# Kernel optimization log

Measured on AMD Instinct MI355X. Metric: run time of the kernel, lower is better.

Reference implementation:

```python
import jax, jax.numpy as jnp
import numpy as np

DISPS = (8, 8, 4, 2)
STRIDES = (2, 1, 1, 1)
DG = 4      # deformable groups
PAD = 1     # (kernel_size-1)//2 for k=3
KH = KW = 3


def pointwise_corr(f1, f2, disp, stride):
    """Windowed pointwise cross-correlation.
    f1, f2: [B, C, H, W]. Returns [B, (2d+1)^2, H, W], dy-major shift order,
    displacement step = stride, normalized by channel count.
    """
    B, C, H, W = f1.shape
    pad = disp * stride
    f2p = jnp.pad(f2, ((0, 0), (0, 0), (pad, pad), (pad, pad)))
    rng = np.arange(2 * disp + 1) * stride
    shifts = np.stack(np.meshgrid(rng, rng, indexing='ij'), -1).reshape(-1, 2)
    shifts = jnp.asarray(shifts, jnp.int32)

    def one(s):
        f2s = jax.lax.dynamic_slice(f2p, (0, 0, s[0], s[1]), (B, C, H, W))
        return jnp.sum(f1 * f2s, axis=1) / C   # [B, H, W]

    corr = jax.vmap(one)(shifts)               # [K2, B, H, W]
    return jnp.transpose(corr, (1, 0, 2, 3))


def bilinear_sample(img, y, x):
    """img: [cg, H, W]; y, x: [K2, H, W] float sample coords.
    Zero outside boundaries (deform-conv semantics). Returns [cg, K2, H, W]."""
    cg, H, W = img.shape
    y0 = jnp.floor(y); x0 = jnp.floor(x)
    wy = y - y0;       wx = x - x0
    y0i = y0.astype(jnp.int32); x0i = x0.astype(jnp.int32)

    def gather(iy, ix):
        valid = (iy >= 0) & (iy < H) & (ix >= 0) & (ix < W)
        v = img[:, jnp.clip(iy, 0, H - 1), jnp.clip(ix, 0, W - 1)]  # [cg,K2,H,W]
        return v * valid.astype(img.dtype)

    v00 = gather(y0i,     x0i)
    v01 = gather(y0i,     x0i + 1)
    v10 = gather(y0i + 1, x0i)
    v11 = gather(y0i + 1, x0i + 1)
    return (v00 * (1 - wy) * (1 - wx) + v01 * (1 - wy) * wx
            + v10 * wy * (1 - wx) + v11 * wy * wx)


def deform_conv(x, offset, weight, dg, pad):
    """Deformable conv v1, stride 1. x: [N,C,H,W]; offset: [N, dg*2*K2, H, W]
    (per group, per kernel point, (dy,dx)); weight: [O, C, kh, kw]."""
    N, C, H, W = x.shape
    O, _, kh, kw = weight.shape
    K2 = kh * kw
    cg = C // dg
    off = offset.reshape(N, dg, K2, 2, H, W)
    ky, kx = np.meshgrid(np.arange(kh), np.arange(kw), indexing='ij')
    ky = jnp.asarray(ky.reshape(-1), jnp.float32)
    kx = jnp.asarray(kx.reshape(-1), jnp.float32)
    gy = jnp.arange(H, dtype=jnp.float32)
    gx = jnp.arange(W, dtype=jnp.float32)
    base_y = ky[:, None, None] - pad + gy[None, :, None]   # [K2,H,1]
    base_x = kx[:, None, None] - pad + gx[None, None, :]   # [K2,1,W]
    ys = base_y[None, None] + off[:, :, :, 0]              # [N,dg,K2,H,W]
    xs = base_x[None, None] + off[:, :, :, 1]
    xg = x.reshape(N, dg, cg, H, W)
    sampled = jax.vmap(jax.vmap(bilinear_sample))(xg, ys, xs)  # [N,dg,cg,K2,H,W]
    w = weight.reshape(O, dg, cg, K2)
    return jnp.einsum('ogck,ngckhw->nohw', w, sampled)


def _forward_single(x, w_off, w_adapt, disp, stride):
    T, B, C, H, W = x.shape
    corrs = [pointwise_corr(x[t], x[t - 1], disp, stride) for t in range(1, T)]
    corr = jnp.concatenate(corrs, axis=0)                   # [(T-1)*B, K2, H, W]
    offset = jnp.einsum('ok,bkhw->bohw', w_off, corr)       # 1x1 conv, no bias
    feat_in = x[1:].reshape((T - 1) * B, C, H, W)
    feat = jax.nn.relu(deform_conv(feat_in, offset, w_adapt, DG, PAD))
    return jnp.concatenate([x[0], feat], axis=0)            # [T*B, C, H, W]


def setup_inputs() -> dict:
    key = jax.random.key(0)
    ks = jax.random.split(key, 12)
    shapes = [(2, 2, 256, 64, 64), (2, 2, 256, 32, 32),
              (2, 2, 256, 16, 16), (2, 2, 256, 8, 8)]
    d = {}
    for i, s in enumerate(shapes):
        d[f"x{i}"] = jax.random.normal(ks[i], s, jnp.float32)
    for i, disp in enumerate(DISPS):
        K2 = (2 * disp + 1) ** 2
        d[f"w_off{i}"] = 0.01 * jax.random.normal(ks[4 + i], (DG * 2 * KH * KW, K2), jnp.float32)
        d[f"w_adapt{i}"] = 0.01 * jax.random.normal(ks[8 + i], (256, 256, KH, KW), jnp.float32)
    return d


def reference(x0, x1, x2, x3, w_off0, w_off1, w_off2, w_off3,
              w_adapt0, w_adapt1, w_adapt2, w_adapt3):
    xs = [x0, x1, x2, x3]
    w_offs = [w_off0, w_off1, w_off2, w_off3]
    w_adapts = [w_adapt0, w_adapt1, w_adapt2, w_adapt3]
    outs = [_forward_single(xs[l], w_offs[l], w_adapts[l], DISPS[l], STRIDES[l])
            for l in range(4)]
    return tuple(outs)
```

## Files before the change

### kernel.cpp

```cpp
#include <hip/hip_runtime.h>

typedef unsigned int u32;
typedef unsigned short u16;
typedef _Float16 f16x2 __attribute__((ext_vector_type(2)));
typedef _Float16 f16x8 __attribute__((ext_vector_type(8)));
typedef __bf16 bf16x8 __attribute__((ext_vector_type(8)));
typedef float f32x4 __attribute__((ext_vector_type(4)));

static __device__ __forceinline__ f16x2 bch(u32 u) { return __builtin_bit_cast(f16x2, u); }


__global__ __launch_bounds__(256) void prep_kernel(
    const float* __restrict__ x0, const float* __restrict__ x1,
    const float* __restrict__ x2, const float* __restrict__ x3,
    const float* __restrict__ w0, const float* __restrict__ w1,
    const float* __restrict__ w2, const float* __restrict__ w3,
    u32* __restrict__ xq, u16* __restrict__ A, float* __restrict__ offs,
    float* __restrict__ out)
{
  __shared__ u32 plds[32 * 65];
  int bx = blockIdx.x, t = threadIdx.x;
  if (bx < 3060) {
    int i = bx * 256 + t;
    if (i < 783360) offs[i] = 0.f;
    return;
  }
  if (bx < 4420) {
    int local = bx - 3060;
    const float* xs; int lvlb, lgW, lgnch;
    if (local < 1024)      { xs = x0; lvlb = 0;       lgW = 6; lgnch = 6; }
    else if (local < 1280) { xs = x1; lvlb = 2097152; lgW = 5; lgnch = 4; local -= 1024; }
    else if (local < 1344) { xs = x2; lvlb = 2621440; lgW = 4; lgnch = 2; local -= 1280; }
    else                   { xs = x3; lvlb = 2752512; lgW = 3; lgnch = 0; local -= 1344; }
    int HW = 1 << (2 * lgW);
    int hc = local & ((1 << lgnch) - 1);
    int g  = (local >> lgnch) & 3;
    int tb = local >> (lgnch + 2);
    int hw0 = hc * 64;
    int lane = t & 63, qd = t >> 6;
#pragma unroll
    for (int j = 0; j < 8; ++j) {
      int cpw = qd * 8 + j;
      int c = tb * 256 + g * 64 + cpw * 2;
      const float* s = xs + (size_t)c * HW + hw0 + lane;
      float f0 = s[0], f1 = s[HW];
      f16x2 h; h[0] = (_Float16)f0; h[1] = (_Float16)f1;
      plds[cpw * 65 + lane] = __builtin_bit_cast(u32, h);
    }
    __syncthreads();
    u32* dst = xq + lvlb + (size_t)(tb * 4 + g) * HW * 32 + (size_t)hw0 * 32;
#pragma unroll
    for (int j = 0; j < 8; ++j) {
      int ow = j * 256 + t;
      int hwl = ow >> 5, ww = ow & 31;
      dst[(size_t)hwl * 32 + ww] = plds[ww * 65 + hwl];
    }
    return;
  }
  if (bx < 13636) {
    int i = (bx - 4420) * 256 + t;
    if (i >= 2359296) return;
    int lv = i / 589824;
    const float* w = (lv == 0) ? w0 : (lv == 1) ? w1 : (lv == 2) ? w2 : w3;
    int local = i - lv * 589824;
    int o = local / 2304;
    int k = local - o * 2304;
    int g = k / 576;
    int r = k - g * 576;
    int p = r >> 6;
    int c = r & 63;
    float v = w[(size_t)(o * 256 + g * 64 + c) * 9 + p];
    __bf16 bv = (__bf16)v;
    A[i] = __builtin_bit_cast(u16, bv);
    return;
  }
  {
    int i = (bx - 13636) * 256 + t;
    const float* xs; int base, dstb;
    if (i < 2097152)      { xs = x0; base = 0;       dstb = 0; }
    else if (i < 2621440) { xs = x1; base = 2097152; dstb = 4194304; }
    else if (i < 2752512) { xs = x2; base = 2621440; dstb = 5242880; }
    else if (i < 2785280) { xs = x3; base = 2752512; dstb = 5505024; }
    else return;
    int local = i - base;
    out[(size_t)dstb + local] = xs[local];
  }
}

__global__ __launch_bounds__(256) void corr_mfma_kernel(const u32* __restrict__ xq, float* __restrict__ corr)
{
  __shared__ __align__(16) u32 lds[8192];
  int t = threadIdx.x, bx = blockIdx.x;

  if (bx >= 1472) {
    int gw = ((bx - 1472) * 256 + t) >> 6;
    int lane = t & 63;
    int cs = lane >> 4, hwi = lane & 15;
    int obase = gw * 16;
    int K2, R, DISP, lgW, xqlb, crb, rel;
    if (obase < 41472)      { K2 = 81; R = 9; DISP = 4; lgW = 4; xqlb = 2621440; crb = 2959360; rel = obase; }
    else if (obase < 44672) { K2 = 25; R = 5; DISP = 2; lgW = 3; xqlb = 2752512; crb = 3000832; rel = obase - 41472; }
    else return;
    int W = 1 << lgW, HW = W * W;
    int hw = (rel & (HW - 1)) + hwi;
    int rr = rel >> (2 * lgW);
    int k = rr % K2, b = rr / K2;
    int h = hw >> lgW, wc = hw & (W - 1);
    int dy = k / R - DISP, dx = k % R - DISP;
    int h2 = h + dy, w2 = wc + dx;
    float a = 0.f;
    if ((u32)h2 < (u32)W && (u32)w2 < (u32)W) {
      const u32* q1 = xq + xqlb + ((size_t)((2 + b) * 4 + cs) * HW + hw) * 32;
      const u32* q0 = xq + xqlb + ((size_t)(b * 4 + cs) * HW + (h2 * W + w2)) * 32;
#pragma unroll 8
      for (int j = 0; j < 32; ++j)
        a = __builtin_amdgcn_fdot2(bch(q1[j]), bch(q0[j]), a, false);
    }
    a += __shfl_xor(a, 16);
    a += __shfl_xor(a, 32);
    if (cs == 0) corr[crb + rel + hwi] = a * 0.00390625f;
    return;
  }

  int sbx = (bx & 7) * 184 + (bx >> 3);
  int l = t & 63, w = t >> 6;
  int lvl, b, y, kq, lgW, W, HW, xqlb, crb;
  if (sbx < 1152) { lvl = 0; int r = sbx;        kq = r % 9; r /= 9; y = r & 63; b = r >> 6;
                    lgW = 6; W = 64; HW = 4096; xqlb = 0;       crb = 0; }
  else            { lvl = 1; int r = sbx - 1152; kq = r % 5; r /= 5; y = r & 31; b = r >> 5;
                    lgW = 5; W = 32; HW = 1024; xqlb = 2097152; crb = 2367488; }
  int par, qy, storeok;
  if (lvl == 0) { int rr = w >> 1; par = w & 1; qy = (kq < 8) ? 2 * kq + rr : 16;
                  storeok = !(kq == 8 && w >= 2); }
  else          { par = 0; qy = 4 * kq + w; storeok = (qy <= 16); if (qy > 16) qy = 16; }
  int rowY = (lvl == 0) ? (y + 2 * qy - 16) : (y + qy - 8);
  int f1words = (lvl == 0) ? 1024 : 512;
  int tb1 = 2 + b, tb0 = b;

  bool f1do = (lvl == 0) || (w < 2);
  u32 f1_lo; int f1_dw;
  {
    int G = w * 64 + l;
    int px = G >> 2, s = G & 3;
    int i = px & 31;
    int pari = px >> 5;
    int x = (lvl == 0) ? (2 * i + pari) : px;
    int cg = (s ^ ((i & 3) ^ ((i >> 2) & 3))) & 3;
    f1_lo = (u32)(xqlb + (y * W + x) * 32 + cg * 4);
    f1_dw = w * 256;
  }
  u32 f2_lo[3], f2_mask[3]; int f2_dw[3];
#pragma unroll
  for (int q = 0; q < 3; ++q) {
    int F = q * 64 + l;
    int jp = F >> 2, s = F & 3;
    int cg = (s ^ ((jp & 3) ^ ((jp >> 2) & 3))) & 3;
    int xs = (lvl == 0) ? (2 * (jp - 8) + par) : (jp - 8);
    bool valid = ((u32)xs < (u32)W) && ((u32)rowY < (u32)W);
    f2_lo[q]   = valid ? (u32)(xqlb + (rowY * W + xs) * 32 + cg * 4) : 6968960u;
    f2_mask[q] = valid ? 0xFFFFFFFFu : 0u;
    f2_dw[q]   = f1words + w * 768 + q * 256;
  }
  int lr = l & 15, lk = l >> 4;
  int aoff[2], boff[3];
#pragma unroll
  for (int it = 0; it < 2; ++it) {
    int iA = it * 16 + lr;
    int px = ((lvl == 0) ? par * 32 : 0) + iA;
    int phys = (lk ^ ((iA & 3) ^ ((iA >> 2) & 3))) & 3;
    aoff[it] = (px * 16 + phys * 4) * 4;
  }
#pragma unroll
  for (int T = 0; T < 3; ++T) {
    int jp = T * 16 + lr;
    int phys = (lk ^ ((jp & 3) ^ ((jp >> 2) & 3))) & 3;
    boff[T] = (f1words + w * 768 + jp * 16 + phys * 4) * 4;
  }

  f32x4 acc0 = {0,0,0,0}, acc1 = {0,0,0,0}, acc2 = {0,0,0,0}, acc3 = {0,0,0,0};

  auto issue = [&](int ch, int sel) {
    int g2 = ch >> 1, hf = ch & 1;
    u32 cb1 = ((u32)(tb1 * 4 + g2) * (u32)HW) * 32u + (u32)hf * 16u;
    u32 cb0 = ((u32)(tb0 * 4 + g2) * (u32)HW) * 32u + (u32)hf * 16u;
    u32* lb = &lds[sel * 4096];
    if (f1do)
      __builtin_amdgcn_global_load_lds(xq + cb1 + f1_lo, lb + f1_dw, 16, 0, 0);
#pragma unroll
    for (int q = 0; q < 3; ++q)
      __builtin_amdgcn_global_load_lds(xq + ((cb0 & f2_mask[q]) + f2_lo[q]), lb + f2_dw[q], 16, 0, 0);
  };

  issue(0, 0);
#pragma unroll 1
  for (int ch = 0; ch < 8; ++ch) {
    int sel = ch & 1;
    asm volatile("s_waitcnt vmcnt(0)" ::: "memory");
    asm volatile("s_barrier" ::: "memory");
    __builtin_amdgcn_sched_barrier(0);
    if (ch < 7) issue(ch + 1, sel ^ 1);
    const char* lb = (const char*)&lds[sel * 4096];
    f16x8 A0 = *(const f16x8*)(lb + aoff[0]);
    f16x8 A1 = *(const f16x8*)(lb + aoff[1]);
    f16x8 B0 = *(const f16x8*)(lb + boff[0]);
    f16x8 B1 = *(const f16x8*)(lb + boff[1]);
    f16x8 B2 = *(const f16x8*)(lb + boff[2]);
    acc0 = __builtin_amdgcn_mfma_f32_16x16x32_f16(A0, B0, acc0, 0, 0, 0);
    acc1 = __builtin_amdgcn_mfma_f32_16x16x32_f16(A0, B1, acc1, 0, 0, 0);
    acc2 = __builtin_amdgcn_mfma_f32_16x16x32_f16(A1, B1, acc2, 0, 0, 0);
    acc3 = __builtin_amdgcn_mfma_f32_16x16x32_f16(A1, B2, acc3, 0, 0, 0);
  }

  if (!storeok) return;
  const float sc = 0.00390625f;
#pragma unroll
  for (int tile = 0; tile < 4; ++tile) {
    int it = (tile >= 2) ? 1 : 0;
    int T  = (tile == 0) ? 0 : (tile == 3) ? 2 : 1;
    f32x4 av = (tile == 0) ? acc0 : (tile == 1) ? acc1 : (tile == 2) ? acc2 : acc3;
    int jp = T * 16 + lr;
#pragma unroll
    for (int jj = 0; jj < 4; ++jj) {
      int i = it * 16 + lk * 4 + jj;
      int qx = jp - i;
      if (qx >= 0 && qx <= 16) {
        int xo = (lvl == 0) ? (2 * i + par) : i;
        int k = qy * 17 + qx;
        corr[crb + (size_t)(b * 289 + k) * HW + y * W + xo] = av[jj] * sc;
      }
    }
  }
}

__global__ __launch_bounds__(256) void offset_kernel(
    const float* __restrict__ corr,
    const float* __restrict__ wo0, const float* __restrict__ wo1,
    const float* __restrict__ wo2, const float* __restrict__ wo3,
    float* __restrict__ offs)
{
  int t = threadIdx.x, bx = blockIdx.x;
  int kc = bx % 6;
  int unit = bx / 6;
  int og = unit & 3;
  int pb = unit >> 2;

  int lgW, K2, crb, ofb, pbl;
  const float* wo;
  if (pb < 32)      { pbl = pb;      lgW = 6; K2 = 289; crb = 0;       ofb = 0;      wo = wo0; }
  else if (pb < 40) { pbl = pb - 32; lgW = 5; K2 = 289; crb = 2367488; ofb = 589824; wo = wo1; }
  else if (pb < 42) { pbl = pb - 40; lgW = 4; K2 = 81;  crb = 2959360; ofb = 737280; wo = wo2; }
  else              { pbl = 0;       lgW = 3; K2 = 25;  crb = 3000832; ofb = 774144; wo = wo3; }
  int HW = 1 << (2 * lgW);
  int pxg = pbl * 256 + t;
  if (lgW == 3 && t >= 128) return;
  int b = pxg >> (2 * lgW);
  int hw = pxg & (HW - 1);

  int kchunk = (K2 + 5) / 6;
  int klo = kc * kchunk;
  int khi = klo + kchunk; if (khi > K2) khi = K2;
  if (klo >= khi) return;

  const float* cr = corr + crb + (size_t)b * K2 * HW + hw;
  const float* wp = wo + (size_t)og * 18 * K2;
  float acc[18];
#pragma unroll
  for (int j = 0; j < 18; ++j) acc[j] = 0.f;
#pragma unroll 2
  for (int k = klo; k < khi; ++k) {
    float cv = cr[(size_t)k * HW];
#pragma unroll
    for (int j = 0; j < 18; ++j) acc[j] = fmaf(wp[(size_t)j * K2 + k], cv, acc[j]);
  }
  float* op = offs + ofb + ((size_t)b * 72 + og * 18) * HW + hw;
#pragma unroll
  for (int j = 0; j < 18; ++j) atomicAdd(&op[(size_t)j * HW], acc[j]);
}

__global__ __launch_bounds__(256) void sample_kernel(
    const u32* __restrict__ xq, const float* __restrict__ offs,
    u16* __restrict__ Bbuf, int Rg0, int nrows)
{
  int bx = blockIdx.x, nbk = gridDim.x;
  int bxs = ((nbk & 7) == 0) ? ((bx & 7) * (nbk >> 3) + (bx >> 3)) : bx;
  int tid = bxs * 256 + threadIdx.x;
  if (tid >= nrows * 144) return;
  int r_l = tid / 144;
  int rem = tid - r_l * 144;
  int gp = rem >> 2, cq = rem & 3;
  int Rg = Rg0 + r_l;
  int b, hw, lgW, xqlb, ofb;
  if (Rg < 8192)       { b = Rg >> 12;       hw = Rg & 4095;  lgW = 6; xqlb = 0;       ofb = 0; }
  else if (Rg < 10240) { int r = Rg - 8192;  b = r >> 10; hw = r & 1023; lgW = 5; xqlb = 2097152; ofb = 589824; }
  else if (Rg < 10752) { int r = Rg - 10240; b = r >> 8;  hw = r & 255;  lgW = 4; xqlb = 2621440; ofb = 737280; }
  else                 { int r = Rg - 10752; b = r >> 6;  hw = r & 63;   lgW = 3; xqlb = 2752512; ofb = 774144; }
  int W = 1 << lgW, HW = W * W;
  u16* rowp = Bbuf + (size_t)r_l * 2304;

  size_t ob = (size_t)ofb + ((size_t)b * 72 + gp * 2) * HW + hw;
  float ody = offs[ob], odx = offs[ob + HW];
  int g = gp / 9, p = gp - g * 9;
  int ky = p / 3, kx = p - ky * 3;
  int sh = hw >> lgW, sw = hw & (W - 1);
  float ys = (float)(sh + ky - 1) + ody;
  float xs = (float)(sw + kx - 1) + odx;
  float y0f = floorf(ys), x0f = floorf(xs);
  float wy = ys - y0f, wx = xs - x0f;
  int y0 = (int)y0f, x0 = (int)x0f, y1 = y0 + 1, x1 = x0 + 1;
  bool vy0 = (u32)y0 < (u32)W, vy1 = (u32)y1 < (u32)W;
  bool vx0 = (u32)x0 < (u32)W, vx1 = (u32)x1 < (u32)W;
  float w00 = (1.f - wy) * (1.f - wx), w01 = (1.f - wy) * wx;
  float w10 = wy * (1.f - wx), w11 = wy * wx;
  const u32* base = xq + xqlb + ((size_t)((2 + b) * 4 + g) * HW) * 32 + cq * 8;
  const uint4 z = make_uint4(0, 0, 0, 0);
  uint4 a00 = z, c00 = z, a01 = z, c01 = z, a10 = z, c10 = z, a11 = z, c11 = z;
  if (vy0 && vx0) { const u32* p0 = base + (size_t)(y0 * W + x0) * 32; a00 = *(const uint4*)p0; c00 = *(const uint4*)(p0 + 4); }
  if (vy0 && vx1) { const u32* p0 = base + (size_t)(y0 * W + x1) * 32; a01 = *(const uint4*)p0; c01 = *(const uint4*)(p0 + 4); }
  if (vy1 && vx0) { const u32* p0 = base + (size_t)(y1 * W + x0) * 32; a10 = *(const uint4*)p0; c10 = *(const uint4*)(p0 + 4); }
  if (vy1 && vx1) { const u32* p0 = base + (size_t)(y1 * W + x1) * 32; a11 = *(const uint4*)p0; c11 = *(const uint4*)(p0 + 4); }
  bf16x8 r0, r1;
#pragma unroll
  for (int ww = 0; ww < 4; ++ww) {
    f16x2 h00 = bch(((const u32*)&a00)[ww]);
    f16x2 h01 = bch(((const u32*)&a01)[ww]);
    f16x2 h10 = bch(((const u32*)&a10)[ww]);
    f16x2 h11 = bch(((const u32*)&a11)[ww]);
    float lo = w00 * (float)h00[0] + w01 * (float)h01[0] + w10 * (float)h10[0] + w11 * (float)h11[0];
    float hi = w00 * (float)h00[1] + w01 * (float)h01[1] + w10 * (float)h10[1] + w11 * (float)h11[1];
    r0[2 * ww] = (__bf16)lo; r0[2 * ww + 1] = (__bf16)hi;
  }
#pragma unroll
  for (int ww = 0; ww < 4; ++ww) {
    f16x2 h00 = bch(((const u32*)&c00)[ww]);
    f16x2 h01 = bch(((const u32*)&c01)[ww]);
    f16x2 h10 = bch(((const u32*)&c10)[ww]);
    f16x2 h11 = bch(((const u32*)&c11)[ww]);
    float lo = w00 * (float)h00[0] + w01 * (float)h01[0] + w10 * (float)h10[0] + w11 * (float)h11[0];
    float hi = w00 * (float)h00[1] + w01 * (float)h01[1] + w10 * (float)h10[1] + w11 * (float)h11[1];
    r1[2 * ww] = (__bf16)lo; r1[2 * ww + 1] = (__bf16)hi;
  }
  u16* dst = rowp + gp * 64 + cq * 16;
  *(bf16x8*)dst = r0;
  *(bf16x8*)(dst + 8) = r1;
}

#define G_ISSUE(P, kt) { const uint4* as_ = (const uint4*)(Asrc + (kt) * 64); \
                         const uint4* bs_ = (const uint4*)(Bsrc + (kt) * 64); \
                         a0##P = as_[0]; a1##P = as_[1]; b0##P = bs_[0]; b1##P = bs_[1]; }
#define G_COMMIT(P, sel) { *(uint4*)(&Al[sel][srow * 72 + sc4 * 16]) = a0##P; \
                           *(uint4*)(&Al[sel][srow * 72 + sc4 * 16 + 8]) = a1##P; \
                           *(uint4*)(&Bl[sel][srow * 72 + sc4 * 16]) = b0##P; \
                           *(uint4*)(&Bl[sel][srow * 72 + sc4 * 16 + 8]) = b1##P; }
#define G_MFMA(sel) { _Pragma("unroll") \
  for (int kk = 0; kk < 2; ++kk) { \
    bf16x8 fb0 = *(const bf16x8*)(&Bl[sel][(wvc * 32 + lr) * 72 + kk * 32 + lk * 8]); \
    bf16x8 fb1 = *(const bf16x8*)(&Bl[sel][(wvc * 32 + 16 + lr) * 72 + kk * 32 + lk * 8]); \
    bf16x8 fa0 = *(const bf16x8*)(&Al[sel][(wvr * 32 + lr) * 72 + kk * 32 + lk * 8]); \
    bf16x8 fa1 = *(const bf16x8*)(&Al[sel][(wvr * 32 + 16 + lr) * 72 + kk * 32 + lk * 8]); \
    acc[0][0] = __builtin_amdgcn_mfma_f32_16x16x32_bf16(fa0, fb0, acc[0][0], 0, 0, 0); \
    acc[0][1] = __builtin_amdgcn_mfma_f32_16x16x32_bf16(fa0, fb1, acc[0][1], 0, 0, 0); \
    acc[1][0] = __builtin_amdgcn_mfma_f32_16x16x32_bf16(fa1, fb0, acc[1][0], 0, 0, 0); \
    acc[1][1] = __builtin_amdgcn_mfma_f32_16x16x32_bf16(fa1, fb1, acc[1][1], 0, 0, 0); \
  } }

__global__ __launch_bounds__(256) void gemm2_kernel(
    const u16* __restrict__ A, const u16* __restrict__ Bbuf,
    int Rg0, float* __restrict__ out)
{
  __shared__ __align__(16) u16 Al[2][64 * 72];
  __shared__ __align__(16) u16 Bl[2][64 * 72];
  int t = threadIdx.x, bx = blockIdx.x;
  int nb = gridDim.x;
  int gsw = (bx & 7) * (nb >> 3) + (bx >> 3);
  int mt = gsw & 3, nt = gsw >> 2;
  int Rgt = Rg0 + nt * 64;
  int b, hw0, lgW, Ab, outb;
  if (Rgt < 8192)       { b = Rgt >> 12;       hw0 = Rgt & 4095;  lgW = 6; Ab = 0;       outb = 2097152; }
  else if (Rgt < 10240) { int r = Rgt - 8192;  b = r >> 10; hw0 = r & 1023; lgW = 5; Ab = 589824;  outb = 4718592; }
  else if (Rgt < 10752) { int r = Rgt - 10240; b = r >> 8;  hw0 = r & 255;  lgW = 4; Ab = 1179648; outb = 5373952; }
  else                  { int r = Rgt - 10752; b = r >> 6;  hw0 = r & 63;   lgW = 3; Ab = 1769472; outb = 5537792; }
  int HW = 1 << (2 * lgW);
  const u16* Bbase = Bbuf + (size_t)(Rgt - Rg0) * 2304;

  int o0 = mt * 64;
  int l = t & 63, wv = t >> 6;
  int lr = l & 15, lk = l >> 4;
  int wvr = wv >> 1, wvc = wv & 1;

  int srow = t >> 2, sc4 = t & 3;
  const u16* Asrc = A + Ab + (size_t)(o0 + srow) * 2304 + sc4 * 16;
  const u16* Bsrc = Bbase + (size_t)srow * 2304 + sc4 * 16;

  f32x4 acc[2][2];
#pragma unroll
  for (int i = 0; i < 2; ++i)
#pragma unroll
    for (int j = 0; j < 2; ++j) acc[i][j] = (f32x4){0, 0, 0, 0};

  uint4 a0A, a1A, b0A, b1A, a0B, a1B, b0B, b1B;

  G_ISSUE(A, 0); G_COMMIT(A, 0);
  G_ISSUE(B, 1);
  G_ISSUE(A, 2);
  __syncthreads();
#pragma unroll 1
  for (int k2 = 0; k2 < 18; ++k2) {
    int kt = 2 * k2;
    G_MFMA(0);
    if (kt < 35) G_COMMIT(B, 1);
    __syncthreads();
    if (kt + 3 < 36) G_ISSUE(B, kt + 3);
    G_MFMA(1);
    if (kt + 1 < 35) G_COMMIT(A, 0);
    __syncthreads();
    if (kt + 4 < 36) G_ISSUE(A, kt + 4);
  }

  float* op = out + outb + (size_t)b * 256 * HW;
#pragma unroll
  for (int ar = 0; ar < 2; ++ar)
#pragma unroll
    for (int bc = 0; bc < 2; ++bc)
#pragma unroll
      for (int j = 0; j < 4; ++j) {
        int orow = o0 + wvr * 32 + ar * 16 + lk * 4 + j;
        int col = hw0 + wvc * 32 + bc * 16 + lr;
        op[(size_t)orow * HW + col] = fmaxf(acc[ar][bc][j], 0.f);
      }
}

extern "C" void kernel_launch(void* const* d_in, const int* in_sizes, int n_in,
                              void* d_out, int out_size, void* d_ws, size_t ws_size,
                              hipStream_t stream) {
  const float* x[4];
  const float* woff[4];
  const float* wad[4];
  for (int l = 0; l < 4; ++l) {
    x[l]    = (const float*)d_in[l];
    woff[l] = (const float*)d_in[4 + 2 * l];
    wad[l]  = (const float*)d_in[5 + 2 * l];
  }
  float* out = (float*)d_out;
  char* ws = (char*)d_ws;
  u32*   xq   = (u32*)(ws);
  u16*   A    = (u16*)(ws + 11141120);
  float* corr = (float*)(ws + 15859712);
  float* offs = (float*)(ws + 27875840);
  u16* BbufS = (u16*)(ws + 15859712);
  u16* BbufL = (u16*)(ws + 31009280);
  int big = (ws_size >= (size_t)81144320) ? 1 : 0;

  prep_kernel<<<24516, 256, 0, stream>>>(x[0], x[1], x[2], x[3],
                                         wad[0], wad[1], wad[2], wad[3], xq, A, offs, out);
  corr_mfma_kernel<<<2170, 256, 0, stream>>>(xq, corr);
  offset_kernel<<<1032, 256, 0, stream>>>(corr, woff[0], woff[1], woff[2], woff[3], offs);

  if (big) {
    sample_kernel<<<6120, 256, 0, stream>>>(xq, offs, BbufL, 0, 10880);
    gemm2_kernel<<<680, 256, 0, stream>>>(A, BbufL, 0, out);
  } else {
    for (int ph = 0; ph < 5; ++ph) {
      int Rg0 = ph * 2560;
      int nrows = (ph < 4) ? 2560 : 640;
      int sgrid = (nrows * 144 + 255) / 256;
      int ggrid = (nrows / 64) * 4;
      sample_kernel<<<sgrid, 256, 0, stream>>>(xq, offs, BbufS, Rg0, nrows);
      gemm2_kernel<<<ggrid, 256, 0, stream>>>(A, BbufS, Rg0, out);
    }
  }
}
```

Measured before the change: 121.7 us.

## Coalesce weight repack via LDS, vectorize copy, split offset K further

The weight repack to bf16 now has each block load one contiguous 576-float row slice into shared memory and transpose it there, replacing the old strided per-element gathers. The passthrough copy of x into the output now uses float4 loads and stores, which cuts the prep grid size. The offset kernel splits the K2 reduction into 12 chunks instead of 6, doubling its blocks for more parallelism at the cost of more atomic adds.

```diff
diff --git a/kernel.cpp b/kernel.cpp
--- a/kernel.cpp
+++ b/kernel.cpp
@@ -57,33 +57,45 @@
     }
     return;
   }
-  if (bx < 13636) {
-    int i = (bx - 4420) * 256 + t;
-    if (i >= 2359296) return;
-    int lv = i / 589824;
+  if (bx < 8516) {
+    int u = bx - 4420;
+    int lv = u >> 10;
+    int rest = u & 1023;
+    int o = rest >> 2, g = rest & 3;
     const float* w = (lv == 0) ? w0 : (lv == 1) ? w1 : (lv == 2) ? w2 : w3;
-    int local = i - lv * 589824;
-    int o = local / 2304;
-    int k = local - o * 2304;
-    int g = k / 576;
-    int r = k - g * 576;
-    int p = r >> 6;
-    int c = r & 63;
-    float v = w[(size_t)(o * 256 + g * 64 + c) * 9 + p];
-    __bf16 bv = (__bf16)v;
-    A[i] = __builtin_bit_cast(u16, bv);
+    const float* src = w + (size_t)(o * 256 + g * 64) * 9;
+    float* fl = (float*)plds;
+    if (t < 256) { fl[t] = src[t]; fl[t + 256] = src[t + 256]; }
+    if (t < 64)  { fl[t + 512] = src[t + 512]; }
+    __syncthreads();
+    u16* dst = A + (size_t)lv * 589824 + (size_t)o * 2304 + g * 576;
+    if (t < 256) {
+#pragma unroll
+      for (int j = 0; j < 2; ++j) {
+        int i = t + j * 256;
+        int c = i & 63, p = i >> 6;
+        __bf16 bv = (__bf16)fl[c * 9 + p];
+        dst[i] = __builtin_bit_cast(u16, bv);
+      }
+    }
+    if (t < 64) {
+      int i = t + 512;
+      int c = i & 63, p = i >> 6;
+      __bf16 bv = (__bf16)fl[c * 9 + p];
+      dst[i] = __builtin_bit_cast(u16, bv);
+    }
     return;
   }
   {
-    int i = (bx - 13636) * 256 + t;
-    const float* xs; int base, dstb;
-    if (i < 2097152)      { xs = x0; base = 0;       dstb = 0; }
-    else if (i < 2621440) { xs = x1; base = 2097152; dstb = 4194304; }
-    else if (i < 2752512) { xs = x2; base = 2621440; dstb = 5242880; }
-    else if (i < 2785280) { xs = x3; base = 2752512; dstb = 5505024; }
+    int i = (bx - 8516) * 256 + t;
+    const float* xs; int base4, dst4;
+    if (i < 524288)      { xs = x0; base4 = 0;      dst4 = 0; }
+    else if (i < 655360) { xs = x1; base4 = 524288; dst4 = 1048576; }
+    else if (i < 688128) { xs = x2; base4 = 655360; dst4 = 1310720; }
+    else if (i < 696320) { xs = x3; base4 = 688128; dst4 = 1376256; }
     else return;
-    int local = i - base;
-    out[(size_t)dstb + local] = xs[local];
+    int local = i - base4;
+    ((float4*)out)[(size_t)dst4 + local] = ((const float4*)xs)[local];
   }
 }
 
@@ -239,8 +251,8 @@
     float* __restrict__ offs)
 {
   int t = threadIdx.x, bx = blockIdx.x;
-  int kc = bx % 6;
-  int unit = bx / 6;
+  int kc = bx % 12;
+  int unit = bx / 12;
   int og = unit & 3;
   int pb = unit >> 2;
 
@@ -256,7 +268,7 @@
   int b = pxg >> (2 * lgW);
   int hw = pxg & (HW - 1);
 
-  int kchunk = (K2 + 5) / 6;
+  int kchunk = (K2 + 11) / 12;
   int klo = kc * kchunk;
   int khi = klo + kchunk; if (khi > K2) khi = K2;
   if (klo >= khi) return;
@@ -450,10 +462,10 @@
   u16* BbufL = (u16*)(ws + 31009280);
   int big = (ws_size >= (size_t)81144320) ? 1 : 0;
 
-  prep_kernel<<<24516, 256, 0, stream>>>(x[0], x[1], x[2], x[3],
+  prep_kernel<<<11236, 256, 0, stream>>>(x[0], x[1], x[2], x[3],
                                          wad[0], wad[1], wad[2], wad[3], xq, A, offs, out);
   corr_mfma_kernel<<<2170, 256, 0, stream>>>(xq, corr);
-  offset_kernel<<<1032, 256, 0, stream>>>(corr, woff[0], woff[1], woff[2], woff[3], offs);
+  offset_kernel<<<2064, 256, 0, stream>>>(corr, woff[0], woff[1], woff[2], woff[3], offs);
 
   if (big) {
     sample_kernel<<<6120, 256, 0, stream>>>(xq, offs, BbufL, 0, 10880);
```

Result: slower. 128.4 us (+5.5%).
